# Kernel optimization log

Measured on AMD Instinct MI355X. Metric: run time of the kernel, lower is better.

The kernel has to match this reference:

```python
import jax, jax.numpy as jnp
import numpy as np

N_LAYERS = 2        # f_aux_layer_num
DIM = 512           # aux_dim
HEADS = 8           # aux_attn_num
HEAD = DIM // HEADS # 64 == aux_attn_dim
FFN_H = int(DIM * 2.0)  # ffn_factor = 2.0 -> 1024
BLOCK = 64          # f_block_size n
L_BLOCKS = 32
M = BLOCK + 1       # block + router token
EPS = 1e-5
THETA = 10000.0


def rms_norm(x, w):
    return x * jax.lax.rsqrt(jnp.mean(x * x, axis=-1, keepdims=True) + EPS) * w


def rotary(x):
    # x: [b, h, s, a]; matches RotaryEmb: halves rotated with outer(t, inv_freq)
    s, a = x.shape[2], x.shape[3]
    inv_freq = (1.0 / THETA) ** (jnp.arange(0, a, 2, dtype=jnp.float32) / a)
    freqs = jnp.arange(s, dtype=jnp.float32)[:, None] * inv_freq[None, :]  # [s, a/2]
    cos, sin = jnp.cos(freqs), jnp.sin(freqs)
    x1, x2 = jnp.split(x, 2, axis=-1)
    return jnp.concatenate([x1 * cos + x2 * sin, -x1 * sin + x2 * cos], axis=-1)


def setup_inputs() -> dict:
    key = jax.random.key(0)
    ks = jax.random.split(key, 10)
    B = 2
    S = L_BLOCKS * M
    x = jax.random.normal(ks[0], (B, L_BLOCKS * BLOCK, DIM), jnp.float32)
    doc = jnp.sort(jax.random.randint(ks[1], (B, S), 0, 4, dtype=jnp.int32), axis=-1)
    w = 0.02
    return {
        "x": x,
        "doc": doc,
        "router_token": jax.random.normal(ks[2], (DIM,), jnp.float32),
        "attn_w": jax.random.normal(ks[3], (N_LAYERS, DIM, 3 * DIM), jnp.float32) * w,
        "attn_o_w": jax.random.normal(ks[4], (N_LAYERS, DIM, DIM), jnp.float32) * w,
        "ffn_up_w": jax.random.normal(ks[5], (N_LAYERS, DIM, 2 * FFN_H), jnp.float32) * w,
        "ffn_down_w": jax.random.normal(ks[6], (N_LAYERS, FFN_H, DIM), jnp.float32) * w,
        "attn_norm_w": jnp.ones((N_LAYERS, DIM), jnp.float32),
        "ffn_norm_w": jnp.ones((N_LAYERS, DIM), jnp.float32),
    }


def reference(x, doc, router_token, attn_w, attn_o_w, ffn_up_w, ffn_down_w,
              attn_norm_w, ffn_norm_w):
    b = x.shape[0]
    # insert router token after each block: [b, l, n+1, d] -> [b, s, d]
    xb = x.reshape(b, L_BLOCKS, BLOCK, DIM)
    rt = jnp.broadcast_to(router_token, (b, L_BLOCKS, 1, DIM))
    h = jnp.concatenate([xb, rt], axis=2).reshape(b, L_BLOCKS * M, DIM)
    s = h.shape[1]

    # mask_mod_1: block-causal AND same-doc
    blk = jnp.arange(s) // M
    causal = blk[:, None] >= blk[None, :]                       # [s, s]
    mask = causal[None] & (doc[:, :, None] == doc[:, None, :])  # [b, s, s]
    neg = jnp.finfo(h.dtype).min
    scale = 1.0 / jnp.sqrt(jnp.float32(HEAD))

    def split_heads(t):
        return t.reshape(b, s, HEADS, HEAD).transpose(0, 2, 1, 3)

    for i in range(N_LAYERS):
        hn = rms_norm(h, attn_norm_w[i])
        qkv = hn @ attn_w[i]                       # [b, s, 3*dim]
        q, k, v = jnp.split(qkv, 3, axis=-1)
        q, k, v = split_heads(q), split_heads(k), split_heads(v)
        q, k = rotary(q), rotary(k)
        scores = jnp.einsum('bhqa,bhka->bhqk', q, k) * scale
        scores = jnp.where(mask[:, None], scores, neg)
        attn = jax.nn.softmax(scores, axis=-1)
        o = jnp.einsum('bhqk,bhka->bhqa', attn, v)
        o = o.transpose(0, 2, 1, 3).reshape(b, s, DIM)
        h = h + o @ attn_o_w[i]
        hf = rms_norm(h, ffn_norm_w[i])
        u1, u2 = jnp.split(hf @ ffn_up_w[i], 2, axis=-1)
        h = h + (jax.nn.silu(u1) * u2) @ ffn_down_w[i]

    # keep router-token slot of each block: [b, l, d]
    return h.reshape(b, L_BLOCKS, M, DIM)[:, :, -1]
```

## Files before the change

### kernel.cpp

```cpp
#include <hip/hip_runtime.h>
#include <math.h>

#define NB 2
#define LB 32
#define BLKN 64
#define MM 65
#define SS (LB*MM)
#define DD 512
#define NH 8
#define HD 64
#define FFH 1024
#define ROWS (NB*SS)
#define WT_LS 2621440

typedef __attribute__((ext_vector_type(8))) short bf16x8;
typedef __attribute__((ext_vector_type(4))) float f32x4;

__device__ __forceinline__ unsigned short f2bf(float f) {
    union { float f; unsigned u; } v; v.f = f;
    unsigned r = (v.u + 0x7FFFu + ((v.u >> 16) & 1u)) >> 16;
    return (unsigned short)r;
}
__device__ __forceinline__ float bf2f(unsigned short u) {
    union { unsigned u; float f; } v; v.u = ((unsigned)u) << 16; return v.f;
}

__device__ __forceinline__ void gload_lds16(const unsigned short* g, unsigned short* l) {
    __builtin_amdgcn_global_load_lds((const __attribute__((address_space(1))) unsigned int*)g,
                                     (__attribute__((address_space(3))) unsigned int*)l,
                                     16, 0, 0);
}

template <int FIRST>
__global__ __launch_bounds__(256) void rms4_k(const float* __restrict__ hsrc,
                                              const float* __restrict__ x,
                                              const float* __restrict__ rt,
                                              const float* __restrict__ w,
                                              float* __restrict__ hout,
                                              unsigned short* __restrict__ out) {
    int row = blockIdx.x * 4 + (threadIdx.x >> 6);
    int lane = threadIdx.x & 63;
    const float* sp;
    if (FIRST) {
        int s = row % SS, b = row / SS;
        int l = s / MM, j = s % MM;
        sp = (j < BLKN) ? x + ((size_t)(b * LB + l) * BLKN + j) * DD : rt;
    } else {
        sp = hsrc + (size_t)row * DD;
    }
    float4 a = *(const float4*)(sp + lane * 8);
    float4 bq = *(const float4*)(sp + lane * 8 + 4);
    float ss = a.x * a.x + a.y * a.y + a.z * a.z + a.w * a.w
             + bq.x * bq.x + bq.y * bq.y + bq.z * bq.z + bq.w * bq.w;
    #pragma unroll
    for (int off = 32; off; off >>= 1) ss += __shfl_xor(ss, off);
    float r = rsqrtf(ss * (1.0f / 512.0f) + 1e-5f);
    float4 w0 = *(const float4*)(w + lane * 8);
    float4 w1 = *(const float4*)(w + lane * 8 + 4);
    unsigned short o8[8] = {f2bf(a.x * r * w0.x), f2bf(a.y * r * w0.y),
                            f2bf(a.z * r * w0.z), f2bf(a.w * r * w0.w),
                            f2bf(bq.x * r * w1.x), f2bf(bq.y * r * w1.y),
                            f2bf(bq.z * r * w1.z), f2bf(bq.w * r * w1.w)};
    *(bf16x8*)(out + (size_t)row * DD + lane * 8) = *(const bf16x8*)o8;
    if (FIRST) {
        *(float4*)(hout + (size_t)row * DD + lane * 8) = a;
        *(float4*)(hout + (size_t)row * DD + lane * 8 + 4) = bq;
    }
}

__global__ __launch_bounds__(256) void wtrans_all_k(const float* __restrict__ attn_w,
                                                    const float* __restrict__ attn_o_w,
                                                    const float* __restrict__ up_w,
                                                    const float* __restrict__ down_w,
                                                    unsigned short* __restrict__ wt) {
    __shared__ unsigned short T[64][66];
    int wg = blockIdx.x;
    int layer = wg >= 640;
    int r = wg - layer * 640;
    const float* W; int K, N; size_t dstOff; int perm = 0;
    if (r < 192)      { W = attn_w   + (size_t)layer * 512 * 1536; K = 512;  N = 1536; dstOff = 0; }
    else if (r < 256) { W = attn_o_w + (size_t)layer * 512 * 512;  K = 512;  N = 512;  dstOff = 786432;  r -= 192; }
    else if (r < 512) { W = up_w     + (size_t)layer * 512 * 2048; K = 512;  N = 2048; dstOff = 1048576; perm = 1; r -= 256; }
    else              { W = down_w   + (size_t)layer * 1024 * 512; K = 1024; N = 512;  dstOff = 2097152; r -= 512; }
    unsigned short* dst = wt + (size_t)layer * WT_LS + dstOff;
    int ntn = N >> 6;
    int n0 = (r % ntn) * 64, k0 = (r / ntn) * 64;
    int t = threadIdx.x;
    #pragma unroll
    for (int i = 0; i < 16; ++i) {
        int e = t + i * 256;
        int rr = e >> 6, cc = e & 63;
        T[rr][cc] = f2bf(W[(size_t)(k0 + rr) * N + n0 + cc]);
    }
    __syncthreads();
    #pragma unroll
    for (int i = 0; i < 16; ++i) {
        int e = t + i * 256;
        int rr = e >> 6, cc = e & 63;
        int n = n0 + rr;
        int nr = n;
        if (perm) {
            int p = n & 1023;
            nr = ((p >> 4) << 5) | ((n >> 10) << 4) | (p & 15);
        }
        dst[(size_t)nr * K + k0 + cc] = T[cc][rr];
    }
}

template <int ADD, int OBF, int ROPE, int SILU>
__global__ __launch_bounds__(256) void gemm_bf16_k(const unsigned short* __restrict__ A,
                                                   const unsigned short* __restrict__ Wt,
                                                   void* __restrict__ Cp,
                                                   int K, int N) {
    __shared__ unsigned short As[64 * 64];
    __shared__ unsigned short Bs[128 * 64];
    int t = threadIdx.x;
    int lane = t & 63, wv = t >> 6;
    int wm = wv >> 1, wn = wv & 1;
    int rowBase = blockIdx.y * 64, colBase = blockIdx.x * 128;
    int c = lane & 15, g = lane >> 4;
    int sw = (c & 7) << 4;

    f32x4 acc[2][4];
    #pragma unroll
    for (int mt = 0; mt < 2; ++mt)
        #pragma unroll
        for (int nt = 0; nt < 4; ++nt) { f32x4 z = {0, 0, 0, 0}; acc[mt][nt] = z; }

    for (int k0 = 0; k0 < K; k0 += 64) {
        __syncthreads();
        #pragma unroll
        for (int i = 0; i < 2; ++i) {
            int e0 = (i * 4 + wv) * 64;
            int e = e0 + lane;
            int row = e >> 3;
            int kb = ((e & 7) << 4) ^ ((row & 7) << 4);
            gload_lds16(A + (size_t)(rowBase + row) * K + k0 + (kb >> 1), &As[e0 * 8]);
        }
        #pragma unroll
        for (int i = 0; i < 4; ++i) {
            int e0 = (i * 4 + wv) * 64;
            int e = e0 + lane;
            int row = e >> 3;
            int kb = ((e & 7) << 4) ^ ((row & 7) << 4);
            gload_lds16(Wt + (size_t)(colBase + row) * K + k0 + (kb >> 1), &Bs[e0 * 8]);
        }
        __syncthreads();

        bf16x8 af[2][2], bfr[4][2];
        #pragma unroll
        for (int mt = 0; mt < 2; ++mt)
            #pragma unroll
            for (int hf = 0; hf < 2; ++hf)
                af[mt][hf] = *(const bf16x8*)
                    &As[((wm * 32 + mt * 16 + c) * 128 + ((hf * 64 + g * 16) ^ sw)) >> 1];
        #pragma unroll
        for (int nt = 0; nt < 4; ++nt)
            #pragma unroll
            for (int hf = 0; hf < 2; ++hf)
                bfr[nt][hf] = *(const bf16x8*)
                    &Bs[((wn * 64 + nt * 16 + c) * 128 + ((hf * 64 + g * 16) ^ sw)) >> 1];
        __builtin_amdgcn_s_setprio(1);
        #pragma unroll
        for (int mt = 0; mt < 2; ++mt)
            #pragma unroll
            for (int nt = 0; nt < 4; ++nt) {
                acc[mt][nt] = __builtin_amdgcn_mfma_f32_16x16x32_bf16(af[mt][0], bfr[nt][0], acc[mt][nt], 0, 0, 0);
                acc[mt][nt] = __builtin_amdgcn_mfma_f32_16x16x32_bf16(af[mt][1], bfr[nt][1], acc[mt][nt], 0, 0, 0);
            }
        __builtin_amdgcn_s_setprio(0);
    }

    if (ROPE) {
        int sec = (colBase + wn * 64) >> 9;
        if (sec < 2) {
            #pragma unroll
            for (int mt = 0; mt < 2; ++mt)
                #pragma unroll
                for (int j = 0; j < 4; ++j) {
                    int row = rowBase + wm * 32 + mt * 16 + g * 4 + j;
                    int spos = row % SS;
                    #pragma unroll
                    for (int p = 0; p < 2; ++p) {
                        float jj = (float)(c + p * 16);
                        float inv = exp2f(jj * -0.41524101186092030f);
                        float fr = (float)spos * inv;
                        float sn, cs; __sincosf(fr, &sn, &cs);
                        float a = acc[mt][p][j], bb = acc[mt][p + 2][j];
                        acc[mt][p][j] = a * cs + bb * sn;
                        acc[mt][p + 2][j] = -a * sn + bb * cs;
                    }
                }
        }
    }

    #pragma unroll
    for (int mt = 0; mt < 2; ++mt)
        #pragma unroll
        for (int j = 0; j < 4; ++j) {
            int row = rowBase + wm * 32 + mt * 16 + g * 4 + j;
            if (SILU) {
                unsigned short* gr = (unsigned short*)Cp + (size_t)row * 1024;
                #pragma unroll
                for (int ntp = 0; ntp < 2; ++ntp) {
                    int npr = colBase + wn * 64 + ntp * 32;
                    int p = ((npr >> 5) << 4) + c;
                    float u1 = acc[mt][2 * ntp][j];
                    float u2 = acc[mt][2 * ntp + 1][j];
                    gr[p] = f2bf((u1 / (1.0f + __expf(-u1))) * u2);
                }
            } else {
                size_t off = (size_t)row * N + colBase + wn * 64 + c;
                if (OBF) {
                    unsigned short* cr = (unsigned short*)Cp + off;
                    #pragma unroll
                    for (int nt = 0; nt < 4; ++nt) cr[nt * 16] = f2bf(acc[mt][nt][j]);
                } else {
                    float* cr = (float*)Cp + off;
                    #pragma unroll
                    for (int nt = 0; nt < 4; ++nt) {
                        if (ADD) cr[nt * 16] += acc[mt][nt][j];
                        else     cr[nt * 16] = acc[mt][nt][j];
                    }
                }
            }
        }
}

#define QR 80

__global__ __launch_bounds__(320) void attn_mfma_k(const unsigned short* __restrict__ qkv,
                                                   const int* __restrict__ doc,
                                                   unsigned short* __restrict__ o) {
    __shared__ unsigned short Qs[QR * 64];
    __shared__ unsigned short Ks[2][64 * 64];
    __shared__ unsigned short Vt[2][64][72];
    __shared__ unsigned short Ps[5][16][72];
    __shared__ int docq[QR];
    __shared__ int dock[2][64];

    int idx = blockIdx.x;
    int l = 31 - (idx >> 4);
    int b = (idx >> 3) & 1;
    int h = idx & 7;
    int t = threadIdx.x;
    int lane = t & 63;
    int wv = t >> 6;

    const unsigned short* qb = qkv + (size_t)b * SS * 1536;
    int rowq0 = l * MM;
    int kmax = (l + 1) * MM;

    #pragma unroll
    for (int it = 0; it < 2; ++it) {
        int ebase = it * 320 + wv * 64;
        int e = ebase + lane;
        int row = e >> 3;
        int kb = ((e & 7) << 4) ^ ((row & 7) << 4);
        int gr = rowq0 + row; if (gr > SS - 1) gr = SS - 1;
        gload_lds16(qb + (size_t)gr * 1536 + h * 64 + (kb >> 1), &Qs[ebase * 8]);
    }
    if (t < QR) docq[t] = (t < MM) ? doc[b * SS + rowq0 + t] : -999999;

    int d0 = doc[b * SS + rowq0];
    int lo = 0, hi = rowq0;
    while (lo < hi) {
        int mid = (lo + hi) >> 1;
        if (doc[b * SS + mid] < d0) lo = mid + 1; else hi = mid;
    }
    int kts = lo >> 6;
    int nkt = (kmax + 63) >> 6;

    const int mt = wv;
    const int g = lane >> 4;
    const int c = lane & 15;
    const int sw = (c & 7) << 4;

    auto stageK = [&](int kbase, int buf) {
        int ebase = wv * 64;
        int e = ebase + lane;
        int row = e >> 3;
        int kb = ((e & 7) << 4) ^ ((row & 7) << 4);
        int kg = kbase + row; if (kg > kmax - 1) kg = kmax - 1;
        gload_lds16(qb + (size_t)kg * 1536 + 512 + h * 64 + (kb >> 1), &Ks[buf][ebase * 8]);
        if (wv < 3) {
            int eb2 = 320 + wv * 64;
            int e2 = eb2 + lane;
            int row2 = e2 >> 3;
            int kb2 = ((e2 & 7) << 4) ^ ((row2 & 7) << 4);
            int kg2 = kbase + row2; if (kg2 > kmax - 1) kg2 = kmax - 1;
            gload_lds16(qb + (size_t)kg2 * 1536 + 512 + h * 64 + (kb2 >> 1), &Ks[buf][eb2 * 8]);
        }
    };
    bf16x8 vr0, vr1; int dnx = 0;
    auto loadV = [&](int kbase) {
        int key = t & 63;
        int de = (t >> 6) * 8;
        int kg = kbase + key; if (kg > kmax - 1) kg = kmax - 1;
        vr0 = *(const bf16x8*)(qb + (size_t)kg * 1536 + 1024 + h * 64 + de);
        if (t < 192) {
            int e2 = 320 + t;
            int key2 = e2 & 63;
            int de2 = (e2 >> 6) * 8;
            int kg2 = kbase + key2; if (kg2 > kmax - 1) kg2 = kmax - 1;
            vr1 = *(const bf16x8*)(qb + (size_t)kg2 * 1536 + 1024 + h * 64 + de2);
        }
        if (t < 64) dnx = (kbase + t < kmax) ? doc[b * SS + kbase + t] : -1000000;
    };
    auto writeV = [&](int buf) {
        int key = t & 63;
        int de = (t >> 6) * 8;
        #pragma unroll
        for (int jj = 0; jj < 8; ++jj) Vt[buf][de + jj][key] = ((unsigned short*)&vr0)[jj];
        if (t < 192) {
            int e2 = 320 + t;
            int key2 = e2 & 63;
            int de2 = (e2 >> 6) * 8;
            #pragma unroll
            for (int jj = 0; jj < 8; ++jj) Vt[buf][de2 + jj][key2] = ((unsigned short*)&vr1)[jj];
        }
        if (t < 64) dock[buf][t] = dnx;
    };

    stageK(kts << 6, 0);
    loadV(kts << 6);
    writeV(0);
    __syncthreads();

    bf16x8 aq[2];
    #pragma unroll
    for (int hf = 0; hf < 2; ++hf)
        aq[hf] = *(const bf16x8*)&Qs[((mt * 16 + c) * 128 + ((hf * 64 + g * 16) ^ sw)) >> 1];
    int dq[4];
    #pragma unroll
    for (int j = 0; j < 4; ++j) dq[j] = docq[mt * 16 + g * 4 + j];

    f32x4 oacc[4];
    float m_[4], l_[4];
    #pragma unroll
    for (int nt = 0; nt < 4; ++nt) { f32x4 z = {0,0,0,0}; oacc[nt] = z; }
    #pragma unroll
    for (int j = 0; j < 4; ++j) { m_[j] = -1e30f; l_[j] = 0.0f; }

    for (int kt = kts; kt < nkt; ++kt) {
        int cur = (kt - kts) & 1;
        bool more = (kt + 1 < nkt);
        if (more) {
            stageK((kt + 1) << 6, cur ^ 1);
            loadV((kt + 1) << 6);
        }

        f32x4 s[4];
        __builtin_amdgcn_s_setprio(1);
        #pragma unroll
        for (int sub = 0; sub < 4; ++sub) {
            f32x4 acc = {0, 0, 0, 0};
            #pragma unroll
            for (int hf = 0; hf < 2; ++hf) {
                bf16x8 bk = *(const bf16x8*)
                    &Ks[cur][((sub * 16 + c) * 128 + ((hf * 64 + g * 16) ^ sw)) >> 1];
                acc = __builtin_amdgcn_mfma_f32_16x16x32_bf16(aq[hf], bk, acc, 0, 0, 0);
            }
            s[sub] = acc;
        }
        __builtin_amdgcn_s_setprio(0);
        #pragma unroll
        for (int sub = 0; sub < 4; ++sub) {
            int dk = dock[cur][sub * 16 + c];
            #pragma unroll
            for (int j = 0; j < 4; ++j)
                s[sub][j] = (dq[j] == dk) ? s[sub][j] * 0.125f : -1e30f;
        }
        float mx[4];
        #pragma unroll
        for (int j = 0; j < 4; ++j)
            mx[j] = fmaxf(fmaxf(s[0][j], s[1][j]), fmaxf(s[2][j], s[3][j]));
        #pragma unroll
        for (int off = 1; off < 16; off <<= 1)
            #pragma unroll
            for (int j = 0; j < 4; ++j) mx[j] = fmaxf(mx[j], __shfl_xor(mx[j], off));
        float mn[4], sc[4], rs[4];
        #pragma unroll
        for (int j = 0; j < 4; ++j) {
            mn[j] = fmaxf(m_[j], mx[j]);
            sc[j] = __expf(m_[j] - mn[j]);
            m_[j] = mn[j];
            rs[j] = 0.0f;
        }
        #pragma unroll
        for (int sub = 0; sub < 4; ++sub)
            #pragma unroll
            for (int j = 0; j < 4; ++j) {
                float p = __expf(s[sub][j] - mn[j]);
                rs[j] += p;
                Ps[wv][g * 4 + j][sub * 16 + c] = f2bf(p);
            }
        #pragma unroll
        for (int off = 1; off < 16; off <<= 1)
            #pragma unroll
            for (int j = 0; j < 4; ++j) rs[j] += __shfl_xor(rs[j], off);
        #pragma unroll
        for (int j = 0; j < 4; ++j) l_[j] = l_[j] * sc[j] + rs[j];
        #pragma unroll
        for (int nt = 0; nt < 4; ++nt)
            #pragma unroll
            for (int j = 0; j < 4; ++j) oacc[nt][j] *= sc[j];
        __builtin_amdgcn_s_setprio(1);
        #pragma unroll
        for (int hf = 0; hf < 2; ++hf) {
            bf16x8 af = *(const bf16x8*)&Ps[wv][c][hf * 32 + g * 8];
            #pragma unroll
            for (int nt = 0; nt < 4; ++nt) {
                bf16x8 bv = *(const bf16x8*)&Vt[cur][nt * 16 + c][hf * 32 + g * 8];
                oacc[nt] = __builtin_amdgcn_mfma_f32_16x16x32_bf16(af, bv, oacc[nt], 0, 0, 0);
            }
        }
        __builtin_amdgcn_s_setprio(0);

        if (more) writeV(cur ^ 1);
        __syncthreads();
    }

    #pragma unroll
    for (int j = 0; j < 4; ++j) {
        int row = mt * 16 + g * 4 + j;
        if (row < MM) {
            float invl = 1.0f / l_[j];
            #pragma unroll
            for (int nt = 0; nt < 4; ++nt)
                o[(size_t)(b * SS + rowq0 + row) * DD + h * 64 + nt * 16 + c] =
                    f2bf(oacc[nt][j] * invl);
        }
    }
}

__global__ void extract_k(const float* __restrict__ h, float* __restrict__ out) {
    int idx = blockIdx.x * blockDim.x + threadIdx.x;
    int d = idx % DD;
    int l = (idx / DD) % LB;
    int b = idx / (DD * LB);
    out[idx] = h[((size_t)(b * SS + l * MM + BLKN)) * DD + d];
}

extern "C" void kernel_launch(void* const* d_in, const int* in_sizes, int n_in,
                              void* d_out, int out_size, void* d_ws, size_t ws_size,
                              hipStream_t stream) {
    const float* x           = (const float*)d_in[0];
    const int*   doc         = (const int*)d_in[1];
    const float* rt          = (const float*)d_in[2];
    const float* attn_w      = (const float*)d_in[3];
    const float* attn_o_w    = (const float*)d_in[4];
    const float* ffn_up_w    = (const float*)d_in[5];
    const float* ffn_down_w  = (const float*)d_in[6];
    const float* attn_norm_w = (const float*)d_in[7];
    const float* ffn_norm_w  = (const float*)d_in[8];
    float* out = (float*)d_out;

    float* h = (float*)d_ws;
    unsigned short* qkvb = (unsigned short*)(h + (size_t)ROWS * 512);
    unsigned short* wt   = qkvb + (size_t)ROWS * 1536;
    unsigned short* hnb  = wt + (size_t)2 * WT_LS;
    unsigned short* ob   = hnb + (size_t)ROWS * 512;
    unsigned short* gb   = ob + (size_t)ROWS * 512;

    wtrans_all_k<<<1280, 256, 0, stream>>>(attn_w, attn_o_w, ffn_up_w, ffn_down_w, wt);

    for (int i = 0; i < 2; ++i) {
        unsigned short* wl = wt + (size_t)i * WT_LS;
        const float* anw = attn_norm_w + (size_t)i * 512;
        const float* fnw = ffn_norm_w  + (size_t)i * 512;

        if (i == 0)
            rms4_k<1><<<ROWS / 4, 256, 0, stream>>>(h, x, rt, anw, h, hnb);
        else
            rms4_k<0><<<ROWS / 4, 256, 0, stream>>>(h, x, rt, anw, h, hnb);
        gemm_bf16_k<0, 1, 1, 0><<<dim3(12, 65), 256, 0, stream>>>(hnb, wl, qkvb, 512, 1536);
        attn_mfma_k<<<512, 320, 0, stream>>>(qkvb, doc, ob);
        gemm_bf16_k<1, 0, 0, 0><<<dim3(4, 65), 256, 0, stream>>>(ob, wl + 786432, h, 512, 512);
        rms4_k<0><<<ROWS / 4, 256, 0, stream>>>(h, x, rt, fnw, h, hnb);
        gemm_bf16_k<0, 0, 0, 1><<<dim3(16, 65), 256, 0, stream>>>(hnb, wl + 1048576, gb, 512, 2048);
        gemm_bf16_k<1, 0, 0, 0><<<dim3(4, 65), 256, 0, stream>>>(gb, wl + 2097152, h, 1024, 512);
    }

    extract_k<<<(NB * LB * DD) / 256, 256, 0, stream>>>(h, out);
}
```

Measured before the change: 226.2 us.

## Enlarge GEMM row tile to 128 and fuse final extraction into last GEMM

The bf16 MFMA GEMM moves from a 64x128 tile to a 128x128 tile, so each wave computes 64 rows and the weight tile loaded into shared memory is reused across twice as many rows. Out-of-range rows are clamped on load and skipped on store, since ROWS is not a multiple of 128. The last down-projection GEMM of layer 2 writes only the router-token rows directly to the output, which removes the separate extract kernel and the full residual write. The trade-off is fewer workgroups (33 row tiles instead of 65), which may lower CU occupancy on the smaller GEMMs, along with higher register pressure.

```diff
diff --git a/kernel.cpp b/kernel.cpp
--- a/kernel.cpp
+++ b/kernel.cpp
@@ -107,35 +107,37 @@
     }
 }
 
-template <int ADD, int OBF, int ROPE, int SILU>
-__global__ __launch_bounds__(256) void gemm_bf16_k(const unsigned short* __restrict__ A,
-                                                   const unsigned short* __restrict__ Wt,
-                                                   void* __restrict__ Cp,
-                                                   int K, int N) {
-    __shared__ unsigned short As[64 * 64];
+template <int ADD, int OBF, int ROPE, int SILU, int FINAL>
+__global__ __launch_bounds__(256) void gemm128_k(const unsigned short* __restrict__ A,
+                                                 const unsigned short* __restrict__ Wt,
+                                                 void* __restrict__ Cp,
+                                                 float* __restrict__ outp,
+                                                 int K, int N) {
+    __shared__ unsigned short As[128 * 64];
     __shared__ unsigned short Bs[128 * 64];
     int t = threadIdx.x;
     int lane = t & 63, wv = t >> 6;
     int wm = wv >> 1, wn = wv & 1;
-    int rowBase = blockIdx.y * 64, colBase = blockIdx.x * 128;
+    int rowBase = blockIdx.y * 128, colBase = blockIdx.x * 128;
     int c = lane & 15, g = lane >> 4;
     int sw = (c & 7) << 4;
 
-    f32x4 acc[2][4];
-    #pragma unroll
-    for (int mt = 0; mt < 2; ++mt)
+    f32x4 acc[4][4];
+    #pragma unroll
+    for (int mt = 0; mt < 4; ++mt)
         #pragma unroll
         for (int nt = 0; nt < 4; ++nt) { f32x4 z = {0, 0, 0, 0}; acc[mt][nt] = z; }
 
     for (int k0 = 0; k0 < K; k0 += 64) {
         __syncthreads();
         #pragma unroll
-        for (int i = 0; i < 2; ++i) {
+        for (int i = 0; i < 4; ++i) {
             int e0 = (i * 4 + wv) * 64;
             int e = e0 + lane;
             int row = e >> 3;
             int kb = ((e & 7) << 4) ^ ((row & 7) << 4);
-            gload_lds16(A + (size_t)(rowBase + row) * K + k0 + (kb >> 1), &As[e0 * 8]);
+            int gr = rowBase + row; if (gr > ROWS - 1) gr = ROWS - 1;
+            gload_lds16(A + (size_t)gr * K + k0 + (kb >> 1), &As[e0 * 8]);
         }
         #pragma unroll
         for (int i = 0; i < 4; ++i) {
@@ -147,13 +149,13 @@
         }
         __syncthreads();
 
-        bf16x8 af[2][2], bfr[4][2];
-        #pragma unroll
-        for (int mt = 0; mt < 2; ++mt)
+        bf16x8 af[4][2], bfr[4][2];
+        #pragma unroll
+        for (int mt = 0; mt < 4; ++mt)
             #pragma unroll
             for (int hf = 0; hf < 2; ++hf)
                 af[mt][hf] = *(const bf16x8*)
-                    &As[((wm * 32 + mt * 16 + c) * 128 + ((hf * 64 + g * 16) ^ sw)) >> 1];
+                    &As[((wm * 64 + mt * 16 + c) * 128 + ((hf * 64 + g * 16) ^ sw)) >> 1];
         #pragma unroll
         for (int nt = 0; nt < 4; ++nt)
             #pragma unroll
@@ -162,7 +164,7 @@
                     &Bs[((wn * 64 + nt * 16 + c) * 128 + ((hf * 64 + g * 16) ^ sw)) >> 1];
         __builtin_amdgcn_s_setprio(1);
         #pragma unroll
-        for (int mt = 0; mt < 2; ++mt)
+        for (int mt = 0; mt < 4; ++mt)
             #pragma unroll
             for (int nt = 0; nt < 4; ++nt) {
                 acc[mt][nt] = __builtin_amdgcn_mfma_f32_16x16x32_bf16(af[mt][0], bfr[nt][0], acc[mt][nt], 0, 0, 0);
@@ -175,10 +177,10 @@
         int sec = (colBase + wn * 64) >> 9;
         if (sec < 2) {
             #pragma unroll
-            for (int mt = 0; mt < 2; ++mt)
+            for (int mt = 0; mt < 4; ++mt)
                 #pragma unroll
                 for (int j = 0; j < 4; ++j) {
-                    int row = rowBase + wm * 32 + mt * 16 + g * 4 + j;
+                    int row = rowBase + wm * 64 + mt * 16 + g * 4 + j;
                     int spos = row % SS;
                     #pragma unroll
                     for (int p = 0; p < 2; ++p) {
@@ -195,10 +197,11 @@
     }
 
     #pragma unroll
-    for (int mt = 0; mt < 2; ++mt)
+    for (int mt = 0; mt < 4; ++mt)
         #pragma unroll
         for (int j = 0; j < 4; ++j) {
-            int row = rowBase + wm * 32 + mt * 16 + g * 4 + j;
+            int row = rowBase + wm * 64 + mt * 16 + g * 4 + j;
+            if (row >= ROWS) continue;
             if (SILU) {
                 unsigned short* gr = (unsigned short*)Cp + (size_t)row * 1024;
                 #pragma unroll
@@ -215,6 +218,15 @@
                     unsigned short* cr = (unsigned short*)Cp + off;
                     #pragma unroll
                     for (int nt = 0; nt < 4; ++nt) cr[nt * 16] = f2bf(acc[mt][nt][j]);
+                } else if (FINAL) {
+                    int s = row % SS;
+                    if (s % MM == BLKN) {
+                        const float* cr = (const float*)Cp + off;
+                        int bb = row / SS, ll = s / MM;
+                        float* orow = outp + ((size_t)(bb * LB + ll)) * DD + colBase + wn * 64 + c;
+                        #pragma unroll
+                        for (int nt = 0; nt < 4; ++nt) orow[nt * 16] = cr[nt * 16] + acc[mt][nt][j];
+                    }
                 } else {
                     float* cr = (float*)Cp + off;
                     #pragma unroll
@@ -434,14 +446,6 @@
     }
 }
 
-__global__ void extract_k(const float* __restrict__ h, float* __restrict__ out) {
-    int idx = blockIdx.x * blockDim.x + threadIdx.x;
-    int d = idx % DD;
-    int l = (idx / DD) % LB;
-    int b = idx / (DD * LB);
-    out[idx] = h[((size_t)(b * SS + l * MM + BLKN)) * DD + d];
-}
-
 extern "C" void kernel_launch(void* const* d_in, const int* in_sizes, int n_in,
                               void* d_out, int out_size, void* d_ws, size_t ws_size,
                               hipStream_t stream) {
@@ -474,13 +478,14 @@
             rms4_k<1><<<ROWS / 4, 256, 0, stream>>>(h, x, rt, anw, h, hnb);
         else
             rms4_k<0><<<ROWS / 4, 256, 0, stream>>>(h, x, rt, anw, h, hnb);
-        gemm_bf16_k<0, 1, 1, 0><<<dim3(12, 65), 256, 0, stream>>>(hnb, wl, qkvb, 512, 1536);
+        gemm128_k<0, 1, 1, 0, 0><<<dim3(12, 33), 256, 0, stream>>>(hnb, wl, qkvb, nullptr, 512, 1536);
         attn_mfma_k<<<512, 320, 0, stream>>>(qkvb, doc, ob);
-        gemm_bf16_k<1, 0, 0, 0><<<dim3(4, 65), 256, 0, stream>>>(ob, wl + 786432, h, 512, 512);
+        gemm128_k<1, 0, 0, 0, 0><<<dim3(4, 33), 256, 0, stream>>>(ob, wl + 786432, h, nullptr, 512, 512);
         rms4_k<0><<<ROWS / 4, 256, 0, stream>>>(h, x, rt, fnw, h, hnb);
-        gemm_bf16_k<0, 0, 0, 1><<<dim3(16, 65), 256, 0, stream>>>(hnb, wl + 1048576, gb, 512, 2048);
-        gemm_bf16_k<1, 0, 0, 0><<<dim3(4, 65), 256, 0, stream>>>(gb, wl + 2097152, h, 1024, 512);
-    }
-
-    extract_k<<<(NB * LB * DD) / 256, 256, 0, stream>>>(h, out);
-}
+        gemm128_k<0, 0, 0, 1, 0><<<dim3(16, 33), 256, 0, stream>>>(hnb, wl + 1048576, gb, nullptr, 512, 2048);
+        if (i == 0)
+            gemm128_k<1, 0, 0, 0, 0><<<dim3(4, 33), 256, 0, stream>>>(gb, wl + 2097152, h, nullptr, 1024, 512);
+        else
+            gemm128_k<1, 0, 0, 0, 1><<<dim3(4, 33), 256, 0, stream>>>(gb, wl + 2097152, h, out, 1024, 512);
+    }
+}
```

Result: slower. 235.0 us (+3.9%).
